# Performance work log

Measured on AMD Instinct MI355X. Metric: run time of the kernel, lower is better.

The kernel has to match this reference:

```python
import jax, jax.numpy as jnp
import numpy as np

# Fano plane lines: for each line (i, j, k) we combine colonies i and j and write to k.
FANO_LINES = np.array([(0, 1, 2), (0, 3, 4), (0, 5, 6), (1, 3, 5), (4, 1, 6), (3, 2, 6), (4, 2, 5)], dtype=np.int32)

B, C, Z = 131072, 7, 64  # batch, colonies (fixed 7), z_dim


def setup_inputs() -> dict:
    key = jax.random.key(0)
    k1, k2, k3 = jax.random.split(key, 3)
    colony_states = jax.random.normal(k1, (B, C, Z), dtype=jnp.float32)
    # nn.Linear(2*z_dim, z_dim): weight [Z, 2Z], bias [Z]
    lim = 1.0 / np.sqrt(2 * Z)
    W = jax.random.uniform(k2, (Z, 2 * Z), dtype=jnp.float32, minval=-lim, maxval=lim)
    b = jax.random.uniform(k3, (Z,), dtype=jnp.float32, minval=-lim, maxval=lim)
    gates = jnp.ones((7,), dtype=jnp.float32) / 7.0  # nn.Parameter init
    return {"colony_states": colony_states, "W": W, "b": b, "gates": gates}


def reference(colony_states, W, b, gates):
    I = jnp.asarray(FANO_LINES[:, 0])
    J = jnp.asarray(FANO_LINES[:, 1])
    K = jnpp = jnp.asarray(FANO_LINES[:, 2])
    g = jax.nn.softmax(gates)  # [7]
    # Vectorized gather over all 7 lines at once: [B, 7, 2Z]
    combined = jnp.concatenate([colony_states[:, I], colony_states[:, J]], axis=-1)
    # Shared linear applied to every line: [B, 7, Z]
    delta = jnp.einsum('blf,zf->blz', combined, W) + b
    gated = g[None, :, None] * delta
    # Gated scatter-add into target colonies; K has duplicates, .add accumulates.
    deltas = jnp.zeros_like(colony_states).at[:, K].add(gated)
    return colony_states + deltas
```

## Files before the change

kernel.cpp:

```cpp
#include <hip/hip_runtime.h>
#include <math.h>


using bf16x8  = __attribute__((ext_vector_type(8))) __bf16;
using floatx4 = __attribute__((ext_vector_type(4))) float;

__device__ __forceinline__ bf16x8 cvt8(floatx4 a, floatx4 b) {
    bf16x8 r;
    r[0]=(__bf16)a[0]; r[1]=(__bf16)a[1]; r[2]=(__bf16)a[2]; r[3]=(__bf16)a[3];
    r[4]=(__bf16)b[0]; r[5]=(__bf16)b[1]; r[6]=(__bf16)b[2]; r[7]=(__bf16)b[3];
    return r;
}

#define LDSF(c, row, slot) ((((c) << 8) | ((row) << 4) | (slot)) << 2)

__global__ __launch_bounds__(256, 3)
void fano_kernel(const float* __restrict__ S,
                 const float* __restrict__ W,
                 const float* __restrict__ bias,
                 const float* __restrict__ gates,
                 float* __restrict__ out, int nt)
{
    __shared__ float buf[2][6144];

    const int tid  = threadIdx.x;
    const int lane = tid & 63;
    const int w    = tid >> 6;
    const int nl   = lane & 15;
    const int qg   = lane >> 4;
    const int bq   = w * 4 + qg;

    float g[7];
    {
        float mx = gates[0];
        #pragma unroll
        for (int i = 1; i < 7; ++i) mx = fmaxf(mx, gates[i]);
        float se = 0.f;
        #pragma unroll
        for (int i = 0; i < 7; ++i) { g[i] = __expf(gates[i] - mx); se += g[i]; }
        const float inv = 1.f / se;
        #pragma unroll
        for (int i = 0; i < 7; ++i) g[i] *= inv;
    }

    const floatx4 bv = *(const floatx4*)(bias + bq * 4);

    bf16x8 wf[4];
    #pragma unroll
    for (int h = 0; h < 4; ++h) {
        const float* p = W + (w * 16 + nl) * 128 + h * 32 + qg * 8;
        wf[h] = cvt8(*(const floatx4*)p, *(const floatx4*)(p + 4));
    }

    long long tile = blockIdx.x;
    if (tile >= nt) return;
    int cur = 0;

    {
        const float* sp = S + tile * 7168 + bq * 448;
        #pragma unroll
        for (int c = 0; c < 6; ++c) {
            floatx4 v = *(const floatx4*)(sp + c * 64 + nl * 4);
            *(floatx4*)(&buf[0][LDSF(c, bq, nl ^ bq)]) = v;
        }
    }
    __syncthreads();

    for (;;) {
        const long long next = tile + gridDim.x;
        const bool more = next < (long long)nt;
        const long long tb = tile * 7168;

        floatx4 stg[6];
        if (more) {
            const float* sp = S + next * 7168 + bq * 448;
            #pragma unroll
            for (int c = 0; c < 6; ++c)
                stg[c] = *(const floatx4*)(sp + c * 64 + nl * 4);
        }
        const floatx4 res6 = *(const floatx4*)(S + tb + nl * 448 + 384 + bq * 4);

        const float* bc = buf[cur];

        floatx4 acc[8];
        #pragma unroll
        for (int s8 = 0; s8 < 8; ++s8) acc[s8] = (floatx4){0.f, 0.f, 0.f, 0.f};
        #pragma unroll
        for (int kb = 0; kb < 2; ++kb) {
            bf16x8 sb[6];
            const int u0 = kb * 8 + qg * 2;
            #pragma unroll
            for (int c = 0; c < 6; ++c) {
                floatx4 f0 = *(const floatx4*)(bc + LDSF(c, nl, (u0    ) ^ nl));
                floatx4 f1 = *(const floatx4*)(bc + LDSF(c, nl, (u0 + 1) ^ nl));
                sb[c] = cvt8(f0, f1);
            }
            acc[0] = __builtin_amdgcn_mfma_f32_16x16x32_bf16(wf[kb],     sb[0], acc[0], 0,0,0);
            acc[1] = __builtin_amdgcn_mfma_f32_16x16x32_bf16(wf[kb],     sb[1], acc[1], 0,0,0);
            acc[2] = __builtin_amdgcn_mfma_f32_16x16x32_bf16(wf[kb],     sb[3], acc[2], 0,0,0);
            acc[3] = __builtin_amdgcn_mfma_f32_16x16x32_bf16(wf[kb],     sb[4], acc[3], 0,0,0);
            acc[4] = __builtin_amdgcn_mfma_f32_16x16x32_bf16(wf[2 + kb], sb[1], acc[4], 0,0,0);
            acc[5] = __builtin_amdgcn_mfma_f32_16x16x32_bf16(wf[2 + kb], sb[2], acc[5], 0,0,0);
            acc[6] = __builtin_amdgcn_mfma_f32_16x16x32_bf16(wf[2 + kb], sb[3], acc[6], 0,0,0);
            acc[7] = __builtin_amdgcn_mfma_f32_16x16x32_bf16(wf[2 + kb], sb[5], acc[7], 0,0,0);
        }

        #pragma unroll
        for (int j = 0; j < 3; ++j) {
            const int c = (j == 2) ? 3 : j;
            floatx4 v = *(const floatx4*)(bc + LDSF(c, bq, nl ^ bq));
            *(floatx4*)(out + tb + bq * 448 + c * 64 + nl * 4) = v;
        }

        const floatx4 r2 = *(const floatx4*)(bc + LDSF(2, nl, bq ^ nl));
        const floatx4 r4 = *(const floatx4*)(bc + LDSF(4, nl, bq ^ nl));
        const floatx4 r5 = *(const floatx4*)(bc + LDSF(5, nl, bq ^ nl));

        floatx4 o2 = r2   + g[0] * (acc[0] + acc[4] + bv);
        floatx4 o4 = r4   + g[1] * (acc[0] + acc[6] + bv);
        floatx4 o5 = r5   + g[3] * (acc[1] + acc[6] + bv)
                          + g[6] * (acc[3] + acc[5] + bv);
        floatx4 o6 = res6 + g[2] * (acc[0] + acc[7] + bv)
                          + g[4] * (acc[3] + acc[4] + bv)
                          + g[5] * (acc[2] + acc[5] + bv);
        float* op = out + tb + nl * 448 + bq * 4;
        *(floatx4*)(op + 2 * 64) = o2;
        *(floatx4*)(op + 4 * 64) = o4;
        *(floatx4*)(op + 5 * 64) = o5;
        *(floatx4*)(op + 6 * 64) = o6;

        if (more) {
            float* bn = buf[cur ^ 1];
            #pragma unroll
            for (int c = 0; c < 6; ++c)
                *(floatx4*)(bn + LDSF(c, bq, nl ^ bq)) = stg[c];
        }
        __syncthreads();
        if (!more) break;
        tile = next;
        cur ^= 1;
    }
}

extern "C" void kernel_launch(void* const* d_in, const int* in_sizes, int n_in,
                              void* d_out, int out_size, void* d_ws, size_t ws_size,
                              hipStream_t stream) {
    const float* S     = (const float*)d_in[0];
    const float* W     = (const float*)d_in[1];
    const float* bias  = (const float*)d_in[2];
    const float* gates = (const float*)d_in[3];
    float* out = (float*)d_out;

    const int B  = in_sizes[0] / (7 * 64);
    const int nt = B / 16;
    int grid = 768;
    if (grid > nt) grid = nt;
    fano_kernel<<<grid, 256, 0, stream>>>(S, W, bias, gates, out, nt);
}
```

Measured before the change: 397.7 us.

## Deepen global prefetch to two tiles ahead and use nontemporal loads/stores

Switches the register prefetch from one tile ahead to two tiles ahead, also prefetching the column-6 residual one tile early. This gives more global loads in flight to hide HBM latency in a bandwidth-bound streaming kernel. It also uses nontemporal loads and stores so the streamed data does not pollute the cache, and issues the pass-through copy stores before the MFMA work. The cost is extra VGPRs for the second staging set, which may reduce occupancy under launch_bounds(256,3).

```diff
diff --git a/kernel.cpp b/kernel.cpp
--- a/kernel.cpp
+++ b/kernel.cpp
@@ -52,6 +52,7 @@
         wf[h] = cvt8(*(const floatx4*)p, *(const floatx4*)(p + 4));
     }
 
+    const long long st = gridDim.x;
     long long tile = blockIdx.x;
     if (tile >= nt) return;
     int cur = 0;
@@ -60,27 +61,48 @@
         const float* sp = S + tile * 7168 + bq * 448;
         #pragma unroll
         for (int c = 0; c < 6; ++c) {
-            floatx4 v = *(const floatx4*)(sp + c * 64 + nl * 4);
+            floatx4 v = __builtin_nontemporal_load((const floatx4*)(sp + c * 64 + nl * 4));
             *(floatx4*)(&buf[0][LDSF(c, bq, nl ^ bq)]) = v;
         }
     }
+    floatx4 stgP[6];
+    if (tile + st < (long long)nt) {
+        const float* sp = S + (tile + st) * 7168 + bq * 448;
+        #pragma unroll
+        for (int c = 0; c < 6; ++c)
+            stgP[c] = __builtin_nontemporal_load((const floatx4*)(sp + c * 64 + nl * 4));
+    }
+    floatx4 res6C = __builtin_nontemporal_load(
+        (const floatx4*)(S + tile * 7168 + nl * 448 + 384 + bq * 4));
     __syncthreads();
 
     for (;;) {
-        const long long next = tile + gridDim.x;
-        const bool more = next < (long long)nt;
+        const long long nxt1 = tile + st;
+        const long long nxt2 = tile + 2 * st;
+        const bool has1 = nxt1 < (long long)nt;
+        const bool has2 = nxt2 < (long long)nt;
         const long long tb = tile * 7168;
 
-        floatx4 stg[6];
-        if (more) {
-            const float* sp = S + next * 7168 + bq * 448;
+        floatx4 stgN[6];
+        if (has2) {
+            const float* sp = S + nxt2 * 7168 + bq * 448;
             #pragma unroll
             for (int c = 0; c < 6; ++c)
-                stg[c] = *(const floatx4*)(sp + c * 64 + nl * 4);
+                stgN[c] = __builtin_nontemporal_load((const floatx4*)(sp + c * 64 + nl * 4));
         }
-        const floatx4 res6 = *(const floatx4*)(S + tb + nl * 448 + 384 + bq * 4);
+        floatx4 res6N;
+        if (has1)
+            res6N = __builtin_nontemporal_load(
+                (const floatx4*)(S + nxt1 * 7168 + nl * 448 + 384 + bq * 4));
 
         const float* bc = buf[cur];
+
+        #pragma unroll
+        for (int j = 0; j < 3; ++j) {
+            const int c = (j == 2) ? 3 : j;
+            floatx4 v = *(const floatx4*)(bc + LDSF(c, bq, nl ^ bq));
+            __builtin_nontemporal_store(v, (floatx4*)(out + tb + bq * 448 + c * 64 + nl * 4));
+        }
 
         floatx4 acc[8];
         #pragma unroll
@@ -105,39 +127,37 @@
             acc[7] = __builtin_amdgcn_mfma_f32_16x16x32_bf16(wf[2 + kb], sb[5], acc[7], 0,0,0);
         }
 
-        #pragma unroll
-        for (int j = 0; j < 3; ++j) {
-            const int c = (j == 2) ? 3 : j;
-            floatx4 v = *(const floatx4*)(bc + LDSF(c, bq, nl ^ bq));
-            *(floatx4*)(out + tb + bq * 448 + c * 64 + nl * 4) = v;
-        }
-
         const floatx4 r2 = *(const floatx4*)(bc + LDSF(2, nl, bq ^ nl));
         const floatx4 r4 = *(const floatx4*)(bc + LDSF(4, nl, bq ^ nl));
         const floatx4 r5 = *(const floatx4*)(bc + LDSF(5, nl, bq ^ nl));
 
-        floatx4 o2 = r2   + g[0] * (acc[0] + acc[4] + bv);
-        floatx4 o4 = r4   + g[1] * (acc[0] + acc[6] + bv);
-        floatx4 o5 = r5   + g[3] * (acc[1] + acc[6] + bv)
-                          + g[6] * (acc[3] + acc[5] + bv);
-        floatx4 o6 = res6 + g[2] * (acc[0] + acc[7] + bv)
-                          + g[4] * (acc[3] + acc[4] + bv)
-                          + g[5] * (acc[2] + acc[5] + bv);
+        floatx4 o2 = r2    + g[0] * (acc[0] + acc[4] + bv);
+        floatx4 o4 = r4    + g[1] * (acc[0] + acc[6] + bv);
+        floatx4 o5 = r5    + g[3] * (acc[1] + acc[6] + bv)
+                           + g[6] * (acc[3] + acc[5] + bv);
+        floatx4 o6 = res6C + g[2] * (acc[0] + acc[7] + bv)
+                           + g[4] * (acc[3] + acc[4] + bv)
+                           + g[5] * (acc[2] + acc[5] + bv);
         float* op = out + tb + nl * 448 + bq * 4;
-        *(floatx4*)(op + 2 * 64) = o2;
-        *(floatx4*)(op + 4 * 64) = o4;
-        *(floatx4*)(op + 5 * 64) = o5;
-        *(floatx4*)(op + 6 * 64) = o6;
+        __builtin_nontemporal_store(o2, (floatx4*)(op + 2 * 64));
+        __builtin_nontemporal_store(o4, (floatx4*)(op + 4 * 64));
+        __builtin_nontemporal_store(o5, (floatx4*)(op + 5 * 64));
+        __builtin_nontemporal_store(o6, (floatx4*)(op + 6 * 64));
 
-        if (more) {
+        if (has1) {
             float* bn = buf[cur ^ 1];
             #pragma unroll
             for (int c = 0; c < 6; ++c)
-                *(floatx4*)(bn + LDSF(c, bq, nl ^ bq)) = stg[c];
+                *(floatx4*)(bn + LDSF(c, bq, nl ^ bq)) = stgP[c];
         }
         __syncthreads();
-        if (!more) break;
-        tile = next;
+        if (!has1) break;
+        if (has2) {
+            #pragma unroll
+            for (int c = 0; c < 6; ++c) stgP[c] = stgN[c];
+        }
+        res6C = res6N;
+        tile = nxt1;
         cur ^= 1;
     }
 }
```

Result: slower. 462.5 us (+16.3%).
